# Kernel tuning notes

Hardware: AMD Instinct MI355X
Metric: run time of the kernel (lower is better)

## Reference

```python
import jax, jax.numpy as jnp
import numpy as np

N_HEADS = 16
N_KV_HEADS = 4
HEAD_DIM = 128
ROPE_THETA = 10000.0


def _rope_cos_sin(seq_len, head_dim, dtype):
    inv_freq = 1.0 / (ROPE_THETA ** (jnp.arange(0, head_dim, 2, dtype=jnp.float32) / head_dim))
    angles = jnp.arange(seq_len, dtype=jnp.float32)[:, None] * inv_freq[None, :]  # [S, hd/2]
    return jnp.cos(angles).astype(dtype), jnp.sin(angles).astype(dtype)


def _apply_rope(t, cos, sin):
    # t: [B, S, H, hd]; interleaved-pair (complex) rotation, Llama style
    B, S, H, hd = t.shape
    tr = t.reshape(B, S, H, hd // 2, 2)
    t0, t1 = tr[..., 0], tr[..., 1]
    c = cos[None, :, None, :]
    s = sin[None, :, None, :]
    out = jnp.stack([t0 * c - t1 * s, t0 * s + t1 * c], axis=-1)
    return out.reshape(B, S, H, hd)


def setup_inputs() -> dict:
    key = jax.random.key(0)
    ks = jax.random.split(key, 5)
    B, S, D = 2, 2048, 2048
    scale = 0.02
    return {
        "x": jax.random.normal(ks[0], (B, S, D), dtype=jnp.float32),
        "wq": jax.random.normal(ks[1], (N_HEADS * HEAD_DIM, D), dtype=jnp.float32) * scale,
        "wk": jax.random.normal(ks[2], (N_KV_HEADS * HEAD_DIM, D), dtype=jnp.float32) * scale,
        "wv": jax.random.normal(ks[3], (N_KV_HEADS * HEAD_DIM, D), dtype=jnp.float32) * scale,
        "wo": jax.random.normal(ks[4], (D, N_HEADS * HEAD_DIM), dtype=jnp.float32) * scale,
    }


def reference(x, wq, wk, wv, wo):
    B, S, D = x.shape
    hd = HEAD_DIM
    # QKV projections (torch Linear: y = x @ W.T)
    q = (x @ wq.T).reshape(B, S, N_HEADS, hd)
    k = (x @ wk.T).reshape(B, S, N_KV_HEADS, hd)
    v = (x @ wv.T).reshape(B, S, N_KV_HEADS, hd)
    # RoPE on q, k
    cos, sin = _rope_cos_sin(S, hd, x.dtype)
    q = _apply_rope(q, cos, sin)
    k = _apply_rope(k, cos, sin)
    # GQA: repeat kv heads to match query heads
    rep = N_HEADS // N_KV_HEADS
    k = jnp.repeat(k, rep, axis=2)  # [B, S, H, hd]
    v = jnp.repeat(v, rep, axis=2)
    # Causal SDPA
    scores = jnp.einsum("bqhd,bkhd->bhqk", q, k) / jnp.sqrt(jnp.asarray(hd, x.dtype))
    causal = jnp.tril(jnp.ones((S, S), dtype=bool))
    scores = jnp.where(causal[None, None], scores, jnp.asarray(-1e30, x.dtype))
    attn = jax.nn.softmax(scores, axis=-1)
    out = jnp.einsum("bhqk,bkhd->bqhd", attn, v).reshape(B, S, N_HEADS * hd)
    return out @ wo.T
```

## Files before the change

kernel.cpp:

```cpp
#include <hip/hip_runtime.h>
#include <stdint.h>

typedef unsigned short u16;
typedef __attribute__((ext_vector_type(8))) __bf16 bf16x8;
typedef __attribute__((ext_vector_type(4))) float f32x4;

__device__ __forceinline__ u16 f2bf(float f) {
  union { float f; uint32_t u; } v; v.f = f;
  uint32_t u = v.u;
  uint32_t r = (u + 0x7fffu + ((u >> 16) & 1u)) >> 16;
  return (u16)r;
}
__device__ __forceinline__ float bf2f(u16 h) {
  union { uint32_t u; float f; } v; v.u = ((uint32_t)h) << 16;
  return v.f;
}

__device__ __forceinline__ void gld16(const void* g, void* l) {
  __builtin_amdgcn_global_load_lds(
      (__attribute__((address_space(1))) void*)(uintptr_t)g,
      (__attribute__((address_space(3))) void*)l,
      16, 0, 0);
}

__global__ __launch_bounds__(256) void cast_all(const float* __restrict__ x,
                                                const float* __restrict__ wq,
                                                const float* __restrict__ wk,
                                                const float* __restrict__ wv,
                                                const float* __restrict__ wo,
                                                u16* __restrict__ xb,
                                                u16* __restrict__ wqkv,
                                                u16* __restrict__ wob) {
  for (int i = blockIdx.x * 256 + threadIdx.x; i < 4718592; i += 2048 * 256) {
    const float* src; u16* dst; int loc, base;
    if (i < 2097152)      { src = x;  dst = xb;   loc = i;           base = 0; }
    else if (i < 3145728) { src = wq; dst = wqkv; loc = i - 2097152; base = 0; }
    else if (i < 3407872) { src = wk; dst = wqkv; loc = i - 3145728; base = 1048576; }
    else if (i < 3670016) { src = wv; dst = wqkv; loc = i - 3407872; base = 1310720; }
    else                  { src = wo; dst = wob;  loc = i - 3670016; base = 0; }
    float4 f = ((const float4*)src)[loc];
    ushort4 o;
    o.x = f2bf(f.x); o.y = f2bf(f.y); o.z = f2bf(f.z); o.w = f2bf(f.w);
    ((ushort4*)dst)[base + loc] = o;
  }
}

__global__ __launch_bounds__(256) void gemm_bt(const u16* __restrict__ A,
                                               const u16* __restrict__ B,
                                               void* __restrict__ C,
                                               u16* __restrict__ Vtg,
                                               int M, int N, int K, int out_f32,
                                               int do_rope)
{
  __shared__ u16 As[128 * 64];
  __shared__ u16 Bs[128 * 64];
  const int tid  = threadIdx.x;
  const int wave = tid >> 6, lane = tid & 63;
  const int col  = lane & 15, quad = lane >> 4;

  const int nwg = gridDim.x * gridDim.y;
  int flat = blockIdx.y * gridDim.x + blockIdx.x;
  int swz  = (nwg & 7) ? flat : ((flat & 7) * (nwg >> 3) + (flat >> 3));
  const int bm = swz / gridDim.x, bn = swz % gridDim.x;

  const int wm = (wave >> 1) * 64, wn = (wave & 1) * 64;
  const size_t arow0 = (size_t)bm * 128, brow0 = (size_t)bn * 128;

  const int sr = lane >> 3, pc = lane & 7;

  const f32x4 fz = {0.f, 0.f, 0.f, 0.f};
  f32x4 acc[4][4];
  for (int i = 0; i < 4; ++i)
    for (int j = 0; j < 4; ++j) acc[i][j] = fz;

  for (int k0 = 0; k0 < K; k0 += 64) {
    __syncthreads();
    #pragma unroll
    for (int i = 0; i < 4; ++i) {
      int rA = wave * 32 + i * 8 + sr;
      int lc = pc ^ (rA & 7);
      gld16(A + (arow0 + rA) * K + k0 + lc * 8, As + (wave * 32 + i * 8) * 64);
      gld16(B + (brow0 + rA) * K + k0 + lc * 8, Bs + (wave * 32 + i * 8) * 64);
    }
    __syncthreads();
    #pragma unroll
    for (int kk = 0; kk < 2; ++kk) {
      const int swzk = (((kk * 4 + quad) ^ (col & 7)) * 8);
      bf16x8 af[4];
      #pragma unroll
      for (int mt = 0; mt < 4; ++mt)
        af[mt] = *(const bf16x8*)&As[(wm + mt * 16 + col) * 64 + swzk];
      #pragma unroll
      for (int nt = 0; nt < 4; ++nt) {
        bf16x8 bf = *(const bf16x8*)&Bs[(wn + nt * 16 + col) * 64 + swzk];
        #pragma unroll
        for (int mt = 0; mt < 4; ++mt)
          acc[mt][nt] = __builtin_amdgcn_mfma_f32_16x16x32_bf16(af[mt], bf, acc[mt][nt], 0, 0, 0);
      }
    }
  }

  const float qscale = 0.12751744515623627f;
  #pragma unroll
  for (int mt = 0; mt < 4; ++mt)
    #pragma unroll
    for (int nt = 0; nt < 4; ++nt) {
      const size_t gcol = brow0 + wn + nt * 16 + col;
      const bool v_here    = do_rope && (gcol >= 2560);
      const bool rope_here = do_rope && (gcol < 2560);
      const int  d    = (int)(gcol & 127);
      const float osc = (gcol < 2048) ? qscale : 1.0f;
      const float inv = exp2f(-(float)(d >> 1) * 0.20762050593046f);
      const bool odd  = (d & 1) != 0;
      if (v_here) {
        const int vc  = (int)gcol - 2560;
        const int kvh = vc >> 7;
        const size_t grow0 = arow0 + wm + mt * 16 + quad * 4;
        const int bb = (int)(grow0 >> 11);
        const int s0 = (int)(grow0 & 2047);
        ushort4 o4;
        o4.x = f2bf(acc[mt][nt][0]);
        o4.y = f2bf(acc[mt][nt][1]);
        o4.z = f2bf(acc[mt][nt][2]);
        o4.w = f2bf(acc[mt][nt][3]);
        *(ushort4*)&Vtg[((size_t)((bb * 4 + kvh) * 128 + d)) * 2048 + s0] = o4;
        continue;
      }
      #pragma unroll
      for (int i = 0; i < 4; ++i) {
        size_t grow = arow0 + wm + mt * 16 + quad * 4 + i;
        float v = acc[mt][nt][i];
        if (rope_here) {
          float p = __shfl_xor(v, 1);
          float ang = (float)(int)(grow & 2047) * inv;
          float sn, cs;
          __sincosf(ang, &sn, &cs);
          v = odd ? (p * sn + v * cs) * osc : (v * cs - p * sn) * osc;
        }
        if (out_f32) ((float*)C)[grow * N + gcol] = v;
        else         ((u16*)C)[grow * N + gcol]   = f2bf(v);
      }
    }
}

__global__ __launch_bounds__(256, 2) void attn_kernel(const u16* __restrict__ QKV,
                                                      const u16* __restrict__ Vtg,
                                                      u16* __restrict__ Ctx,
                                                      int B, int S)
{
  const int x = blockIdx.x;
  const int t = x >> 5, bh = x & 31;
  const int qt = (x < 256) ? (15 - t) : (t - 8);
  const int h = bh & 15, b = bh >> 4;
  const int tid  = threadIdx.x;
  const int wave = tid >> 6, lane = tid & 63;
  const int col  = lane & 15, quad = lane >> 4;
  const int q0   = qt * 128;
  const int kvh  = h >> 2;
  const int row0w = q0 + wave * 32;

  __shared__ u16 Ks[64 * 128];
  __shared__ u16 Vt[128 * 64];
  __shared__ u16 Ps[4][32 * 72];

  bf16x8 aq[2][4];
  #pragma unroll
  for (int mt = 0; mt < 2; ++mt)
    #pragma unroll
    for (int ks = 0; ks < 4; ++ks)
      aq[mt][ks] = *(const bf16x8*)(QKV + (size_t)(b * S + row0w + mt * 16 + col) * 3072
                                        + h * 128 + ks * 32 + quad * 8);

  const u16* KVb = QKV + (size_t)b * S * 3072 + 2048 + kvh * 128;
  const u16* Vtb = Vtg + ((size_t)(b * 4 + kvh) * 128) * S;
  u16* Pw = Ps[wave];

  const f32x4 fz = {0.f, 0.f, 0.f, 0.f};
  f32x4 o[2][8];
  #pragma unroll
  for (int mt = 0; mt < 2; ++mt)
    #pragma unroll
    for (int nc = 0; nc < 8; ++nc) o[mt][nc] = fz;
  float rs[2] = {0.f, 0.f};

  const int kt_max = 2 * qt + 1;

  for (int kt = 0; kt <= kt_max; ++kt) {
    __syncthreads();
    #pragma unroll
    for (int i = 0; i < 4; ++i) {
      int r = wave * 16 + i * 4 + (lane >> 4);
      int lc = (lane & 15) ^ (r & 15);
      gld16(KVb + (size_t)(kt * 64 + r) * 3072 + lc * 8, Ks + (wave * 16 + i * 4) * 128);
    }
    #pragma unroll
    for (int i = 0; i < 4; ++i) {
      int r = wave * 32 + i * 8 + (lane >> 3);
      int lc = (lane & 7) ^ (r & 7);
      gld16(Vtb + (size_t)r * S + kt * 64 + lc * 8, Vt + (wave * 32 + i * 8) * 64);
    }
    __syncthreads();

    if (kt * 64 > row0w + 31) continue;
    const bool need_mask = (kt * 64 + 63 > row0w);

    #pragma unroll
    for (int nt = 0; nt < 4; ++nt) {
      bf16x8 kA[4];
      #pragma unroll
      for (int ks = 0; ks < 4; ++ks)
        kA[ks] = *(const bf16x8*)&Ks[(nt * 16 + col) * 128 + (((ks * 4 + quad) ^ col) * 8)];
      #pragma unroll
      for (int mt = 0; mt < 2; ++mt) {
        f32x4 st = fz;
        #pragma unroll
        for (int ks = 0; ks < 4; ++ks)
          st = __builtin_amdgcn_mfma_f32_16x16x32_bf16(kA[ks], aq[mt][ks], st, 0, 0, 0);
        float pv[4];
        const int kbase = kt * 64 + nt * 16 + quad * 4;
        const int qrow  = row0w + mt * 16 + col;
        #pragma unroll
        for (int i = 0; i < 4; ++i) {
          float s = st[i];
          if (need_mask && (kbase + i > qrow)) s = -__builtin_inff();
          pv[i] = exp2f(s);
        }
        rs[mt] += (pv[0] + pv[1]) + (pv[2] + pv[3]);
        uint32_t d0 = (__float_as_uint(pv[0]) >> 16) | (__float_as_uint(pv[1]) & 0xffff0000u);
        uint32_t d1 = (__float_as_uint(pv[2]) >> 16) | (__float_as_uint(pv[3]) & 0xffff0000u);
        uint2 dd; dd.x = d0; dd.y = d1;
        *(uint2*)&Pw[(mt * 16 + col) * 72 + nt * 16 + quad * 4] = dd;
      }
    }
    __asm__ volatile("" ::: "memory");

    bf16x8 ap[2][2];
    #pragma unroll
    for (int mt = 0; mt < 2; ++mt)
      #pragma unroll
      for (int ks = 0; ks < 2; ++ks)
        ap[mt][ks] = *(const bf16x8*)&Pw[(mt * 16 + col) * 72 + ks * 32 + quad * 8];
    #pragma unroll
    for (int nc = 0; nc < 8; ++nc) {
      #pragma unroll
      for (int ks = 0; ks < 2; ++ks) {
        bf16x8 bv = *(const bf16x8*)&Vt[(nc * 16 + col) * 64 + (((ks * 4 + quad) ^ (col & 7)) * 8)];
        #pragma unroll
        for (int mt = 0; mt < 2; ++mt)
          o[mt][nc] = __builtin_amdgcn_mfma_f32_16x16x32_bf16(ap[mt][ks], bv, o[mt][nc], 0, 0, 0);
      }
    }
  }

  #pragma unroll
  for (int mt = 0; mt < 2; ++mt) {
    float v = rs[mt];
    v += __shfl_xor(v, 16);
    v += __shfl_xor(v, 32);
    float lv[4];
    #pragma unroll
    for (int i = 0; i < 4; ++i)
      lv[i] = 1.0f / __shfl(v, quad * 4 + i);
    #pragma unroll
    for (int nc = 0; nc < 8; ++nc)
      #pragma unroll
      for (int i = 0; i < 4; ++i) {
        int qg = row0w + mt * 16 + quad * 4 + i;
        Ctx[(size_t)(b * S + qg) * 2048 + h * 128 + nc * 16 + col] =
            f2bf(o[mt][nc][i] * lv[i]);
      }
  }
}

extern "C" void kernel_launch(void* const* d_in, const int* in_sizes, int n_in,
                              void* d_out, int out_size, void* d_ws, size_t ws_size,
                              hipStream_t stream) {
  const int B = 2, S = 2048, D = 2048;
  const int M = B * S;
  const int NQKV = 3072;

  const float* x  = (const float*)d_in[0];
  const float* wq = (const float*)d_in[1];
  const float* wk = (const float*)d_in[2];
  const float* wv = (const float*)d_in[3];
  const float* wo = (const float*)d_in[4];

  char* ws = (char*)d_ws;
  u16* xb    = (u16*)ws; ws += (size_t)M * D * 2;
  u16* wqkvb = (u16*)ws; ws += (size_t)NQKV * D * 2;
  u16* wob   = (u16*)ws; ws += (size_t)D * D * 2;
  u16* qkvb  = (u16*)ws; ws += (size_t)M * NQKV * 2;
  u16* vtg   = (u16*)ws; ws += (size_t)B * 4 * 128 * S * 2;
  u16* ctx   = (u16*)ws; ws += (size_t)M * D * 2;

  cast_all<<<2048, 256, 0, stream>>>(x, wq, wk, wv, wo, xb, wqkvb, wob);

  gemm_bt<<<dim3(NQKV / 128, M / 128), 256, 0, stream>>>(xb, wqkvb, qkvb, vtg, M, NQKV, D, 0, 1);

  attn_kernel<<<512, 256, 0, stream>>>(qkvb, vtg, ctx, B, S);

  gemm_bt<<<dim3(D / 128, M / 128), 256, 0, stream>>>(ctx, wob, d_out, vtg, M, D, D, 1, 0);
}
```

Measured before the change: 293.3 us.

## Split-K the output projection and stage V transpose through LDS

The output projection GEMM is split into two K halves along grid z. The second half writes float partials into reused workspace, and a new add kernel sums them into the output; the goal is more workgroups and better CU occupancy. The QKV GEMM's V tiles are transposed through shared memory, so Vt stores become coalesced 8-byte row writes instead of scattered 4-element column writes. The cost is an extra launch plus about 48MB of additional float partial traffic, and the workspace aliasing relies on xb and wqkv no longer being needed by that point.

```diff
diff --git a/kernel.cpp b/kernel.cpp
--- a/kernel.cpp
+++ b/kernel.cpp
@@ -47,13 +47,15 @@
 
 __global__ __launch_bounds__(256) void gemm_bt(const u16* __restrict__ A,
                                                const u16* __restrict__ B,
-                                               void* __restrict__ C,
+                                               void* __restrict__ C0,
+                                               void* __restrict__ C1,
                                                u16* __restrict__ Vtg,
-                                               int M, int N, int K, int out_f32,
-                                               int do_rope)
+                                               int M, int N, int Kstride, int Klen,
+                                               int out_f32, int do_rope)
 {
-  __shared__ u16 As[128 * 64];
-  __shared__ u16 Bs[128 * 64];
+  __shared__ u16 sh[2][128 * 64];
+  u16* const As = sh[0];
+  u16* const Bs = sh[1];
   const int tid  = threadIdx.x;
   const int wave = tid >> 6, lane = tid & 63;
   const int col  = lane & 15, quad = lane >> 4;
@@ -63,6 +65,9 @@
   int swz  = (nwg & 7) ? flat : ((flat & 7) * (nwg >> 3) + (flat >> 3));
   const int bm = swz / gridDim.x, bn = swz % gridDim.x;
 
+  void* const C = (blockIdx.z == 0) ? C0 : C1;
+  const int koff = (int)blockIdx.z * Klen;
+
   const int wm = (wave >> 1) * 64, wn = (wave & 1) * 64;
   const size_t arow0 = (size_t)bm * 128, brow0 = (size_t)bn * 128;
 
@@ -73,14 +78,14 @@
   for (int i = 0; i < 4; ++i)
     for (int j = 0; j < 4; ++j) acc[i][j] = fz;
 
-  for (int k0 = 0; k0 < K; k0 += 64) {
+  for (int k0 = 0; k0 < Klen; k0 += 64) {
     __syncthreads();
     #pragma unroll
     for (int i = 0; i < 4; ++i) {
       int rA = wave * 32 + i * 8 + sr;
       int lc = pc ^ (rA & 7);
-      gld16(A + (arow0 + rA) * K + k0 + lc * 8, As + (wave * 32 + i * 8) * 64);
-      gld16(B + (brow0 + rA) * K + k0 + lc * 8, Bs + (wave * 32 + i * 8) * 64);
+      gld16(A + (arow0 + rA) * Kstride + koff + k0 + lc * 8, As + (wave * 32 + i * 8) * 64);
+      gld16(B + (brow0 + rA) * Kstride + koff + k0 + lc * 8, Bs + (wave * 32 + i * 8) * 64);
     }
     __syncthreads();
     #pragma unroll
@@ -100,32 +105,49 @@
     }
   }
 
-  const float qscale = 0.12751744515623627f;
-  #pragma unroll
-  for (int mt = 0; mt < 4; ++mt)
-    #pragma unroll
-    for (int nt = 0; nt < 4; ++nt) {
-      const size_t gcol = brow0 + wn + nt * 16 + col;
-      const bool v_here    = do_rope && (gcol >= 2560);
-      const bool rope_here = do_rope && (gcol < 2560);
-      const int  d    = (int)(gcol & 127);
-      const float osc = (gcol < 2048) ? qscale : 1.0f;
-      const float inv = exp2f(-(float)(d >> 1) * 0.20762050593046f);
-      const bool odd  = (d & 1) != 0;
-      if (v_here) {
-        const int vc  = (int)gcol - 2560;
-        const int kvh = vc >> 7;
-        const size_t grow0 = arow0 + wm + mt * 16 + quad * 4;
-        const int bb = (int)(grow0 >> 11);
-        const int s0 = (int)(grow0 & 2047);
+  const bool v_block = do_rope && (brow0 >= 2560);
+  if (v_block) {
+    __syncthreads();
+    u16* sc = &sh[0][0];
+    #pragma unroll
+    for (int mt = 0; mt < 4; ++mt)
+      #pragma unroll
+      for (int nt = 0; nt < 4; ++nt) {
+        const int d = wn + nt * 16 + col;
+        const int g = ((wm + mt * 16) >> 2) + quad;
         ushort4 o4;
         o4.x = f2bf(acc[mt][nt][0]);
         o4.y = f2bf(acc[mt][nt][1]);
         o4.z = f2bf(acc[mt][nt][2]);
         o4.w = f2bf(acc[mt][nt][3]);
-        *(ushort4*)&Vtg[((size_t)((bb * 4 + kvh) * 128 + d)) * 2048 + s0] = o4;
-        continue;
-      }
+        *(ushort4*)&sc[d * 128 + ((g ^ (d & 31)) << 2)] = o4;
+      }
+    __syncthreads();
+    const int kvh    = (int)((brow0 - 2560) >> 7);
+    const int bb     = (int)(arow0 >> 11);
+    const int s_base = (int)(arow0 & 2047);
+    u16* vdst = Vtg + ((size_t)(bb * 4 + kvh) * 128) * 2048 + s_base;
+    #pragma unroll
+    for (int pass = 0; pass < 16; ++pass) {
+      int idx = pass * 256 + tid;
+      int d = idx >> 5, g = idx & 31;
+      uint2 val = *(const uint2*)&sc[d * 128 + ((g ^ (d & 31)) << 2)];
+      *(uint2*)&vdst[(size_t)d * 2048 + g * 4] = val;
+    }
+    return;
+  }
+
+  const float qscale = 0.12751744515623627f;
+  #pragma unroll
+  for (int mt = 0; mt < 4; ++mt)
+    #pragma unroll
+    for (int nt = 0; nt < 4; ++nt) {
+      const size_t gcol = brow0 + wn + nt * 16 + col;
+      const bool rope_here = do_rope != 0;
+      const int  d    = (int)(gcol & 127);
+      const float osc = (gcol < 2048) ? qscale : 1.0f;
+      const float inv = exp2f(-(float)(d >> 1) * 0.20762050593046f);
+      const bool odd  = (d & 1) != 0;
       #pragma unroll
       for (int i = 0; i < 4; ++i) {
         size_t grow = arow0 + wm + mt * 16 + quad * 4 + i;
@@ -141,6 +163,16 @@
         else         ((u16*)C)[grow * N + gcol]   = f2bf(v);
       }
     }
+}
+
+__global__ __launch_bounds__(256) void addf(float* __restrict__ out,
+                                            const float* __restrict__ p1, int n4) {
+  for (int i = blockIdx.x * 256 + threadIdx.x; i < n4; i += 2048 * 256) {
+    float4 a = ((float4*)out)[i];
+    float4 b = ((const float4*)p1)[i];
+    a.x += b.x; a.y += b.y; a.z += b.z; a.w += b.w;
+    ((float4*)out)[i] = a;
+  }
 }
 
 __global__ __launch_bounds__(256, 2) void attn_kernel(const u16* __restrict__ QKV,
@@ -288,16 +320,20 @@
   char* ws = (char*)d_ws;
   u16* xb    = (u16*)ws; ws += (size_t)M * D * 2;
   u16* wqkvb = (u16*)ws; ws += (size_t)NQKV * D * 2;
+  u16* vtg   = (u16*)ws; ws += (size_t)B * 4 * 128 * S * 2;
   u16* wob   = (u16*)ws; ws += (size_t)D * D * 2;
   u16* qkvb  = (u16*)ws; ws += (size_t)M * NQKV * 2;
-  u16* vtg   = (u16*)ws; ws += (size_t)B * 4 * 128 * S * 2;
   u16* ctx   = (u16*)ws; ws += (size_t)M * D * 2;
+  float* p1  = (float*)d_ws;
 
   cast_all<<<2048, 256, 0, stream>>>(x, wq, wk, wv, wo, xb, wqkvb, wob);
 
-  gemm_bt<<<dim3(NQKV / 128, M / 128), 256, 0, stream>>>(xb, wqkvb, qkvb, vtg, M, NQKV, D, 0, 1);
+  gemm_bt<<<dim3(NQKV / 128, M / 128, 1), 256, 0, stream>>>(
+      xb, wqkvb, qkvb, nullptr, vtg, M, NQKV, D, D, 0, 1);
 
   attn_kernel<<<512, 256, 0, stream>>>(qkvb, vtg, ctx, B, S);
 
-  gemm_bt<<<dim3(D / 128, M / 128), 256, 0, stream>>>(ctx, wob, d_out, vtg, M, D, D, 1, 0);
-}
+  gemm_bt<<<dim3(D / 128, M / 128, 2), 256, 0, stream>>>(
+      ctx, wob, d_out, p1, nullptr, M, D, D, D / 2, 1, 0);
+  addf<<<2048, 256, 0, stream>>>((float*)d_out, p1, (M * D) / 4);
+}
```

After: 341.4 us. 16.4% more time.

## Add double-buffered LDS GEMM for output projection with swizzled block order

Applied to the files above, without the earlier changes.

Adds a dedicated output-projection GEMM kernel that double-buffers A and B tiles in LDS. The next K-slice is prefetched with global_load_lds while MFMAs run on the current slice, so only one barrier is needed per iteration. It also remaps workgroup indices so consecutive groups share tiles for better L2 reuse. LDS use doubles to 64KB per block, which may reduce occupancy compared with the original kernel.

```diff
diff --git a/kernel.cpp b/kernel.cpp
--- a/kernel.cpp
+++ b/kernel.cpp
@@ -143,6 +143,85 @@
     }
 }
 
+__global__ __launch_bounds__(256) void gemm_bt_dbuf(const u16* __restrict__ A,
+                                                    const u16* __restrict__ B,
+                                                    float* __restrict__ C,
+                                                    int M, int N, int K)
+{
+  __shared__ u16 As[2][128 * 64];
+  __shared__ u16 Bs[2][128 * 64];
+  const int tid  = threadIdx.x;
+  const int wave = tid >> 6, lane = tid & 63;
+  const int col  = lane & 15, quad = lane >> 4;
+
+  const int nwg = gridDim.x * gridDim.y;
+  int flat = blockIdx.y * gridDim.x + blockIdx.x;
+  int swz  = (nwg & 7) ? flat : ((flat & 7) * (nwg >> 3) + (flat >> 3));
+  const int bm = swz / gridDim.x, bn = swz % gridDim.x;
+
+  const int wm = (wave >> 1) * 64, wn = (wave & 1) * 64;
+  const size_t arow0 = (size_t)bm * 128, brow0 = (size_t)bn * 128;
+  const int sr = lane >> 3, pc = lane & 7;
+
+  const f32x4 fz = {0.f, 0.f, 0.f, 0.f};
+  f32x4 acc[4][4];
+  for (int i = 0; i < 4; ++i)
+    for (int j = 0; j < 4; ++j) acc[i][j] = fz;
+
+  #pragma unroll
+  for (int i = 0; i < 4; ++i) {
+    int rA = wave * 32 + i * 8 + sr;
+    int lc = pc ^ (rA & 7);
+    gld16(A + (arow0 + rA) * K + lc * 8, As[0] + (wave * 32 + i * 8) * 64);
+    gld16(B + (brow0 + rA) * K + lc * 8, Bs[0] + (wave * 32 + i * 8) * 64);
+  }
+
+  const int T = K / 64;
+  for (int t = 0; t < T; ++t) {
+    __syncthreads();
+    if (t + 1 < T) {
+      const int k0 = (t + 1) * 64;
+      u16* ad = As[(t + 1) & 1];
+      u16* bd = Bs[(t + 1) & 1];
+      #pragma unroll
+      for (int i = 0; i < 4; ++i) {
+        int rA = wave * 32 + i * 8 + sr;
+        int lc = pc ^ (rA & 7);
+        gld16(A + (arow0 + rA) * K + k0 + lc * 8, ad + (wave * 32 + i * 8) * 64);
+        gld16(B + (brow0 + rA) * K + k0 + lc * 8, bd + (wave * 32 + i * 8) * 64);
+      }
+    }
+    const u16* Ac = As[t & 1];
+    const u16* Bc = Bs[t & 1];
+    #pragma unroll
+    for (int kk = 0; kk < 2; ++kk) {
+      const int swzk = (((kk * 4 + quad) ^ (col & 7)) * 8);
+      bf16x8 af[4];
+      #pragma unroll
+      for (int mt = 0; mt < 4; ++mt)
+        af[mt] = *(const bf16x8*)&Ac[(wm + mt * 16 + col) * 64 + swzk];
+      #pragma unroll
+      for (int nt = 0; nt < 4; ++nt) {
+        bf16x8 bf = *(const bf16x8*)&Bc[(wn + nt * 16 + col) * 64 + swzk];
+        #pragma unroll
+        for (int mt = 0; mt < 4; ++mt)
+          acc[mt][nt] = __builtin_amdgcn_mfma_f32_16x16x32_bf16(af[mt], bf, acc[mt][nt], 0, 0, 0);
+      }
+    }
+  }
+
+  #pragma unroll
+  for (int mt = 0; mt < 4; ++mt)
+    #pragma unroll
+    for (int nt = 0; nt < 4; ++nt)
+      #pragma unroll
+      for (int i = 0; i < 4; ++i) {
+        size_t grow = arow0 + wm + mt * 16 + quad * 4 + i;
+        size_t gcol = brow0 + wn + nt * 16 + col;
+        C[grow * N + gcol] = acc[mt][nt][i];
+      }
+}
+
 __global__ __launch_bounds__(256, 2) void attn_kernel(const u16* __restrict__ QKV,
                                                       const u16* __restrict__ Vtg,
                                                       u16* __restrict__ Ctx,
@@ -299,5 +378,5 @@
 
   attn_kernel<<<512, 256, 0, stream>>>(qkvb, vtg, ctx, B, S);
 
-  gemm_bt<<<dim3(D / 128, M / 128), 256, 0, stream>>>(ctx, wob, d_out, vtg, M, D, D, 1, 0);
-}
+  gemm_bt_dbuf<<<dim3(D / 128, M / 128), 256, 0, stream>>>(ctx, wob, (float*)d_out, M, D, D);
+}
```

Result: faster. 287.3 us (-2.1%).
